# Performance work log

Measured on AMD Instinct MI355X. Metric: run time of the kernel, lower is better.

Reference implementation:

```python
import jax, jax.numpy as jnp
import numpy as np
from jax import lax

BAD = -10000.0
K = 10
W = 512  # window_size


def setup_inputs() -> dict:
    key = jax.random.key(0)
    k1, k2, k3, k4 = jax.random.split(key, 4)
    S, B, P, D, R = 4, 256, 32768, 256, 1000
    return {
        "relation": jax.random.randint(k1, (S, B), 0, R, dtype=jnp.int32),
        "head": jax.random.randint(k2, (S, B), 0, P, dtype=jnp.int32),
        "entity_embedding": jax.random.normal(k3, (S, P, D), dtype=jnp.float32),
        "relation_embedding": jax.random.normal(k4, (R, D), dtype=jnp.float32),
    }


def reference(relation, head, entity_embedding, relation_embedding):
    S, B = relation.shape
    P, D = entity_embedding.shape[1], entity_embedding.shape[2]
    Q = S * B            # total queries after all_gather
    NBEST = K + 1
    n_rep = -(-P // W)   # ceil

    # all_gather of queries across shards (every shard sees all queries)
    rel_all = relation.reshape(-1)                                   # (Q,)
    head_emb_all = entity_embedding[jnp.arange(S)[:, None], head]    # (S,B,D)
    head_emb_all = head_emb_all.reshape(Q, D)
    # DistMult score_tails: <h, r, t> ; fold h*r into one query vector
    qvec = head_emb_all * relation_embedding[rel_all]                # (Q,D)

    init_sc = jnp.full((S, Q, NBEST), BAD, dtype=jnp.float32)
    init_ix = jnp.full((S, Q, NBEST), P, dtype=jnp.int32)

    def step(carry, w):
        sc, ix = carry
        start = w * W
        # local idx of this window, clamped like the torch mask branch
        raw = start + jnp.arange(W, dtype=jnp.int32)                 # (W,)
        valid = raw < P
        slide = jnp.where(valid, raw, P - 1)
        neg = lax.dynamic_slice_in_dim(entity_embedding,
                                       jnp.minimum(start, P - W), W, axis=1)  # (S,W,D)
        scores_w = jnp.einsum('qd,swd->sqw', qvec, neg)              # (S,Q,W)
        scores_w = scores_w + BAD * (~valid).astype(scores_w.dtype)
        all_sc = jnp.concatenate([scores_w, sc], axis=-1)            # (S,Q,W+NBEST)
        all_ix = jnp.concatenate(
            [jnp.broadcast_to(slide, (S, Q, W)), ix], axis=-1)
        top_sc, top_pos = lax.top_k(all_sc, NBEST)
        top_ix = jnp.take_along_axis(all_ix, top_pos, axis=-1)
        return (top_sc, top_ix), None

    (best_sc, best_ix), _ = lax.scan(step, (init_sc, init_ix),
                                     jnp.arange(n_rep, dtype=jnp.int32))

    # all_to_all: (src_shard, dst_shard, bs, nbest) -> (dst, src, bs, nbest)
    best_sc = best_sc.reshape(S, S, B, NBEST).transpose(1, 0, 2, 3)
    best_ix = best_ix.reshape(S, S, B, NBEST).transpose(1, 0, 2, 3)

    # mask out placeholder / padding local indices (shard_counts == P)
    best_sc = best_sc + BAD * (best_ix >= P).astype(best_sc.dtype)

    # shard_and_idx_to_entity: interleaved global ids, padded column for idx==P
    base = jnp.arange(P, dtype=jnp.int32)[None, :] * S \
        + jnp.arange(S, dtype=jnp.int32)[:, None]                    # (S,P)
    table = jnp.concatenate(
        [base, jnp.full((S, 1), -1, dtype=jnp.int32)], axis=1)       # (S,P+1)
    src = jnp.arange(S, dtype=jnp.int32)[None, :, None, None]
    best_gid = table[src, best_ix]                                   # (S,S,B,NBEST)

    # per destination shard: merge the S per-source-shard top-(k+1) lists
    sc_flat = best_sc.transpose(0, 2, 1, 3).reshape(S, B, S * NBEST)
    gid_flat = best_gid.transpose(0, 2, 1, 3).reshape(S, B, S * NBEST)
    topk_sc, topk_pos = lax.top_k(sc_flat, K)                        # (S,B,K)
    topk_gid = jnp.take_along_axis(gid_flat, topk_pos, axis=-1)
    return topk_gid, topk_sc
```

## Files before the change

### kernel.cpp

```cpp
#include <hip/hip_runtime.h>

#define SS 4
#define BB 256
#define PP 32768
#define DD 256
#define QQ 1024
#define NN 131072
#define KTOP 10
#define QTILE 128
#define WQ 32
#define NCHUNK 64
#define CHROWS 2048
#define PANEL 64
#define NPANEL (CHROWS / PANEL)
#define JCH 8
#define MSLOT 20
#define ROWG 33
#define ROWE (ROWG * 8)
#define PANB (PANEL * ROWG * 16)
#define KEYMASK 0xFFFFF800u
#define MWS 132
#define CVB 4096

typedef __attribute__((ext_vector_type(8))) short bf16x8;
typedef __attribute__((ext_vector_type(4))) float f32x4;
typedef __attribute__((ext_vector_type(16))) float f32x16;
typedef __attribute__((ext_vector_type(4))) unsigned int u32x4;

static __device__ __forceinline__ short f2bf(float f) {
    union { float f; unsigned u; } v; v.f = f;
    unsigned r = (v.u + 0x7FFFu + ((v.u >> 16) & 1u)) >> 16;
    return (short)r;
}
static __device__ __forceinline__ bf16x8 cvt8(f32x4 a, f32x4 b) {
    bf16x8 r;
    r[0] = f2bf(a[0]); r[1] = f2bf(a[1]); r[2] = f2bf(a[2]); r[3] = f2bf(a[3]);
    r[4] = f2bf(b[0]); r[5] = f2bf(b[1]); r[6] = f2bf(b[2]); r[7] = f2bf(b[3]);
    return r;
}
static __device__ __forceinline__ unsigned umax(unsigned a, unsigned b) { return a > b ? a : b; }
static __device__ __forceinline__ unsigned umin(unsigned a, unsigned b) { return a < b ? a : b; }

__global__ void prep_kernel(const int* __restrict__ rel, const int* __restrict__ head,
                            const float* __restrict__ E, const float* __restrict__ R,
                            short* __restrict__ Ebf, short* __restrict__ qbf) {
    if (blockIdx.x < CVB) {
        size_t base = ((size_t)blockIdx.x * 256 + threadIdx.x) * 32;
        #pragma unroll
        for (int c = 0; c < 4; c++) {
            f32x4 a = *(const f32x4*)(E + base + c * 8);
            f32x4 b = *(const f32x4*)(E + base + c * 8 + 4);
            *(bf16x8*)(Ebf + base + c * 8) = cvt8(a, b);
        }
    } else {
        int q = blockIdx.x - CVB, d = threadIdx.x;
        int s1 = q >> 8;
        float f = E[((size_t)(s1 * PP + head[q])) * DD + d] * R[(size_t)rel[q] * DD + d];
        qbf[q * DD + d] = f2bf(f);
    }
}

__launch_bounds__(256, 2)
__global__ void score_topk_kernel(const short* __restrict__ Ebf, const short* __restrict__ qbf,
                                  unsigned* __restrict__ parts) {
    __shared__ __align__(16) char smem[2 * PANB];

    const int tid  = threadIdx.x;
    const int wave = tid >> 6;
    const int lane = tid & 63;
    const int lh   = lane >> 5;
    const int ln   = lane & 31;
    const int mtile = blockIdx.x >> 6;
    const int chunk = blockIdx.x & 63;

    short* buf0 = (short*)smem;
    short* buf1 = (short*)(smem + PANB);

    bf16x8 afrag[16];
    {
        const int arow = mtile * QTILE + wave * WQ + ln;
        #pragma unroll
        for (int ks = 0; ks < 16; ks++)
            afrag[ks] = *(const bf16x8*)(qbf + arow * DD + ks * 16 + lh * 8);
    }

    unsigned lst[16][4];
    #pragma unroll
    for (int r = 0; r < 16; r++)
        #pragma unroll
        for (int i = 0; i < 4; i++) lst[r][i] = 0u;

    const int n0c = chunk * CHROWS;

    bf16x8 st[8];
    #pragma unroll
    for (int it = 0; it < 8; it++) {
        int gi = it * 256 + tid, row = gi >> 5, slot = gi & 31;
        st[it] = *(const bf16x8*)(Ebf + (size_t)(n0c + row) * DD + slot * 8);
    }
    #pragma unroll
    for (int it = 0; it < 8; it++) {
        int gi = it * 256 + tid, row = gi >> 5, slot = gi & 31;
        *(bf16x8*)(buf0 + row * ROWE + slot * 8) = st[it];
    }

    for (int p = 0; p < NPANEL; p++) {
        short* bp = (p & 1) ? buf1 : buf0;
        short* bn = (p & 1) ? buf0 : buf1;
        __syncthreads();
        if (p + 1 < NPANEL) {
            const int n1 = n0c + (p + 1) * PANEL;
            #pragma unroll
            for (int it = 0; it < 8; it++) {
                int gi = it * 256 + tid, row = gi >> 5, slot = gi & 31;
                st[it] = *(const bf16x8*)(Ebf + (size_t)(n1 + row) * DD + slot * 8);
            }
        }

        f32x16 acc0, acc1;
        #pragma unroll
        for (int r = 0; r < 16; r++) { acc0[r] = 256.0f; acc1[r] = 256.0f; }
        const short* b0 = bp + ln * ROWE + lh * 8;
        const short* b1 = bp + (32 + ln) * ROWE + lh * 8;
        #pragma unroll
        for (int ks = 0; ks < 16; ks++) {
            bf16x8 x0 = *(const bf16x8*)(b0 + ks * 16);
            bf16x8 x1 = *(const bf16x8*)(b1 + ks * 16);
            acc0 = __builtin_amdgcn_mfma_f32_32x32x16_bf16(afrag[ks], x0, acc0, 0, 0, 0);
            acc1 = __builtin_amdgcn_mfma_f32_32x32x16_bf16(afrag[ks], x1, acc1, 0, 0, 0);
        }

        const unsigned c0 = (unsigned)(p * 64 + ln);
        const unsigned c1 = (unsigned)(p * 64 + 32 + ln);
        #pragma unroll
        for (int r = 0; r < 16; r++) {
            unsigned key = (__float_as_uint(acc0[r]) & KEYMASK) | c0;
            unsigned n0 = umin(umax(key, lst[r][0]), lst[r][1]);
            unsigned n1 = umin(umax(key, lst[r][1]), lst[r][2]);
            unsigned n2 = umin(umax(key, lst[r][2]), lst[r][3]);
            unsigned n3 = umax(key, lst[r][3]);
            lst[r][0] = n0; lst[r][1] = n1; lst[r][2] = n2; lst[r][3] = n3;
        }
        #pragma unroll
        for (int r = 0; r < 16; r++) {
            unsigned key = (__float_as_uint(acc1[r]) & KEYMASK) | c1;
            unsigned n0 = umin(umax(key, lst[r][0]), lst[r][1]);
            unsigned n1 = umin(umax(key, lst[r][1]), lst[r][2]);
            unsigned n2 = umin(umax(key, lst[r][2]), lst[r][3]);
            unsigned n3 = umax(key, lst[r][3]);
            lst[r][0] = n0; lst[r][1] = n1; lst[r][2] = n2; lst[r][3] = n3;
        }

        if (p + 1 < NPANEL) {
            #pragma unroll
            for (int it = 0; it < 8; it++) {
                int gi = it * 256 + tid, row = gi >> 5, slot = gi & 31;
                *(bf16x8*)(bn + row * ROWE + slot * 8) = st[it];
            }
        }
    }

    __syncthreads();
    unsigned* mw = (unsigned*)smem + (size_t)wave * (WQ * MWS);
    #pragma unroll
    for (int r = 0; r < 16; r++) {
        int q = (r & 3) + 8 * (r >> 2) + 4 * lh;
        u32x4 v; v[0] = lst[r][0]; v[1] = lst[r][1]; v[2] = lst[r][2]; v[3] = lst[r][3];
        *(u32x4*)(mw + q * MWS + ln * 4) = v;
    }
    if (lane < 32) {
        unsigned rr[JCH];
        #pragma unroll
        for (int i = 0; i < JCH; i++) rr[i] = 0u;
        #pragma unroll
        for (int j = 0; j < 32; j++) {
            u32x4 v = *(const u32x4*)(mw + lane * MWS + j * 4);
            #pragma unroll
            for (int e = 0; e < 4; e++) {
                unsigned x = v[e];
                unsigned t0 = umin(umax(x, rr[0]), rr[1]);
                unsigned t1 = umin(umax(x, rr[1]), rr[2]);
                unsigned t2 = umin(umax(x, rr[2]), rr[3]);
                unsigned t3 = umin(umax(x, rr[3]), rr[4]);
                unsigned t4 = umin(umax(x, rr[4]), rr[5]);
                unsigned t5 = umin(umax(x, rr[5]), rr[6]);
                unsigned t6 = umin(umax(x, rr[6]), rr[7]);
                unsigned t7 = umax(x, rr[7]);
                rr[0]=t0; rr[1]=t1; rr[2]=t2; rr[3]=t3; rr[4]=t4; rr[5]=t5; rr[6]=t6; rr[7]=t7;
            }
        }
        const int qg = mtile * QTILE + wave * WQ + lane;
        unsigned* dst = parts + ((size_t)qg * NCHUNK + chunk) * JCH;
        #pragma unroll
        for (int i = 0; i < JCH; i++) dst[i] = rr[JCH - 1 - i];
    }
}

__global__ void finalize_kernel(const int* __restrict__ rel, const int* __restrict__ head,
                                const float* __restrict__ E, const float* __restrict__ R,
                                const unsigned* __restrict__ parts, float* __restrict__ out) {
    __shared__ float qv[DD];
    __shared__ int   gl[MSLOT];
    __shared__ float rsc[MSLOT];
    __shared__ int   rgid[MSLOT];

    const int q = blockIdx.x;
    const int tid = threadIdx.x;
    const int wave = tid >> 6, lane = tid & 63;
    const int s1 = q >> 8;

    qv[tid] = E[((size_t)(s1 * PP + head[q])) * DD + tid] * R[(size_t)rel[q] * DD + tid];

    if (wave == 0) {
        unsigned run[JCH];
        const unsigned* src = parts + ((size_t)q * NCHUNK + lane) * JCH;
        #pragma unroll
        for (int j = 0; j < JCH; j++) run[j] = src[j];
        for (int r = 0; r < MSLOT; r++) {
            unsigned best = run[0]; int bl = lane;
            #pragma unroll
            for (int off = 32; off >= 1; off >>= 1) {
                unsigned ob = __shfl_xor(best, off);
                int ol = __shfl_xor(bl, off);
                if (ob > best || (ob == best && ol < bl)) { best = ob; bl = ol; }
            }
            if (lane == bl) {
                int col = (int)(best & 0x7FFu);
                int n = lane * CHROWS + col;
                gl[r] = ((n & (PP - 1)) << 2) | (n >> 15);
                #pragma unroll
                for (int j = 0; j < JCH - 1; j++) run[j] = run[j + 1];
                run[JCH - 1] = 0u;
            }
        }
    }
    __syncthreads();

    f32x4 qq = *(const f32x4*)(qv + lane * 4);
    #pragma unroll
    for (int c = 0; c < MSLOT / 4; c++) {
        int j = wave * (MSLOT / 4) + c;
        int gid = gl[j];
        int n = (gid & 3) * PP + (gid >> 2);
        f32x4 ev = *(const f32x4*)(E + (size_t)n * DD + lane * 4);
        f32x4 p = qq * ev;
        float s = (p[0] + p[1]) + (p[2] + p[3]);
        #pragma unroll
        for (int off = 32; off >= 1; off >>= 1) s += __shfl_xor(s, off);
        if (lane == 0) { rsc[j] = s; rgid[j] = gid; }
    }
    __syncthreads();

    if (tid < 64) {
        float a = (tid < MSLOT) ? rsc[tid] : -1e30f;
        int   g = (tid < MSLOT) ? rgid[tid] : 0;
        for (int r = 0; r < KTOP; r++) {
            float ps = a; int pg = g; int plm = tid;
            #pragma unroll
            for (int off = 32; off >= 1; off >>= 1) {
                float os = __shfl_xor(ps, off);
                int   og = __shfl_xor(pg, off);
                int   ol = __shfl_xor(plm, off);
                if (os > ps || (os == ps && ol < plm)) { ps = os; pg = og; plm = ol; }
            }
            if (tid == 0) {
                out[q * KTOP + r]             = (float)pg;
                out[QQ * KTOP + q * KTOP + r] = ps;
            }
            if (tid == plm) a = -1e30f;
        }
    }
}

extern "C" void kernel_launch(void* const* d_in, const int* in_sizes, int n_in,
                              void* d_out, int out_size, void* d_ws, size_t ws_size,
                              hipStream_t stream) {
    const int*   rel  = (const int*)d_in[0];
    const int*   head = (const int*)d_in[1];
    const float* E    = (const float*)d_in[2];
    const float* R    = (const float*)d_in[3];

    char* ws = (char*)d_ws;
    short* Ebf = (short*)ws;
    short* qbf = (short*)(ws + (size_t)NN * DD * 2);
    unsigned* parts = (unsigned*)(ws + (size_t)NN * DD * 2 + (size_t)QQ * DD * 2);

    prep_kernel<<<dim3(CVB + QQ), dim3(256), 0, stream>>>(rel, head, E, R, Ebf, qbf);
    score_topk_kernel<<<dim3((QQ / QTILE) * NCHUNK), dim3(256), 0, stream>>>(Ebf, qbf, parts);
    finalize_kernel<<<dim3(QQ), dim3(256), 0, stream>>>(rel, head, E, R, parts, (float*)d_out);
}
```

Before: 307.0 us.

## Fuse fp32-to-bf16 entity conversion into the score kernel's panel loads

Drops the separate pass that converted the whole entity table to bf16 in workspace. The score kernel now reads fp32 rows directly and packs them to bf16 by truncation while staging panels into shared memory. This removes a full read plus write of the table and one intermediate buffer. In exchange each of the 8 query-tile blocks per chunk reads twice as many bytes from global memory (fp32 instead of bf16), uses more staging registers, and rounds by truncation instead of round-to-nearest.

```diff
diff --git a/kernel.cpp b/kernel.cpp
--- a/kernel.cpp
+++ b/kernel.cpp
@@ -20,7 +20,6 @@
 #define PANB (PANEL * ROWG * 16)
 #define KEYMASK 0xFFFFF800u
 #define MWS 132
-#define CVB 4096
 
 typedef __attribute__((ext_vector_type(8))) short bf16x8;
 typedef __attribute__((ext_vector_type(4))) float f32x4;
@@ -32,36 +31,29 @@
     unsigned r = (v.u + 0x7FFFu + ((v.u >> 16) & 1u)) >> 16;
     return (short)r;
 }
-static __device__ __forceinline__ bf16x8 cvt8(f32x4 a, f32x4 b) {
-    bf16x8 r;
-    r[0] = f2bf(a[0]); r[1] = f2bf(a[1]); r[2] = f2bf(a[2]); r[3] = f2bf(a[3]);
-    r[4] = f2bf(b[0]); r[5] = f2bf(b[1]); r[6] = f2bf(b[2]); r[7] = f2bf(b[3]);
-    return r;
+static __device__ __forceinline__ unsigned pk2(float lo, float hi) {
+    return (__float_as_uint(hi) & 0xFFFF0000u) | (__float_as_uint(lo) >> 16);
+}
+static __device__ __forceinline__ u32x4 pk8(f32x4 a, f32x4 b) {
+    u32x4 g;
+    g[0] = pk2(a[0], a[1]); g[1] = pk2(a[2], a[3]);
+    g[2] = pk2(b[0], b[1]); g[3] = pk2(b[2], b[3]);
+    return g;
 }
 static __device__ __forceinline__ unsigned umax(unsigned a, unsigned b) { return a > b ? a : b; }
 static __device__ __forceinline__ unsigned umin(unsigned a, unsigned b) { return a < b ? a : b; }
 
-__global__ void prep_kernel(const int* __restrict__ rel, const int* __restrict__ head,
+__global__ void qvec_kernel(const int* __restrict__ rel, const int* __restrict__ head,
                             const float* __restrict__ E, const float* __restrict__ R,
-                            short* __restrict__ Ebf, short* __restrict__ qbf) {
-    if (blockIdx.x < CVB) {
-        size_t base = ((size_t)blockIdx.x * 256 + threadIdx.x) * 32;
-        #pragma unroll
-        for (int c = 0; c < 4; c++) {
-            f32x4 a = *(const f32x4*)(E + base + c * 8);
-            f32x4 b = *(const f32x4*)(E + base + c * 8 + 4);
-            *(bf16x8*)(Ebf + base + c * 8) = cvt8(a, b);
-        }
-    } else {
-        int q = blockIdx.x - CVB, d = threadIdx.x;
-        int s1 = q >> 8;
-        float f = E[((size_t)(s1 * PP + head[q])) * DD + d] * R[(size_t)rel[q] * DD + d];
-        qbf[q * DD + d] = f2bf(f);
-    }
+                            short* __restrict__ qbf) {
+    int q = blockIdx.x, d = threadIdx.x;
+    int s1 = q >> 8;
+    float f = E[((size_t)(s1 * PP + head[q])) * DD + d] * R[(size_t)rel[q] * DD + d];
+    qbf[q * DD + d] = f2bf(f);
 }
 
 __launch_bounds__(256, 2)
-__global__ void score_topk_kernel(const short* __restrict__ Ebf, const short* __restrict__ qbf,
+__global__ void score_topk_kernel(const float* __restrict__ E, const short* __restrict__ qbf,
                                   unsigned* __restrict__ parts) {
     __shared__ __align__(16) char smem[2 * PANB];
 
@@ -92,16 +84,18 @@
 
     const int n0c = chunk * CHROWS;
 
-    bf16x8 st[8];
+    f32x4 sa[8], sb[8];
     #pragma unroll
     for (int it = 0; it < 8; it++) {
         int gi = it * 256 + tid, row = gi >> 5, slot = gi & 31;
-        st[it] = *(const bf16x8*)(Ebf + (size_t)(n0c + row) * DD + slot * 8);
+        const float* src = E + (size_t)(n0c + row) * DD + slot * 8;
+        sa[it] = *(const f32x4*)(src);
+        sb[it] = *(const f32x4*)(src + 4);
     }
     #pragma unroll
     for (int it = 0; it < 8; it++) {
         int gi = it * 256 + tid, row = gi >> 5, slot = gi & 31;
-        *(bf16x8*)(buf0 + row * ROWE + slot * 8) = st[it];
+        *(u32x4*)(buf0 + row * ROWE + slot * 8) = pk8(sa[it], sb[it]);
     }
 
     for (int p = 0; p < NPANEL; p++) {
@@ -113,7 +107,9 @@
             #pragma unroll
             for (int it = 0; it < 8; it++) {
                 int gi = it * 256 + tid, row = gi >> 5, slot = gi & 31;
-                st[it] = *(const bf16x8*)(Ebf + (size_t)(n1 + row) * DD + slot * 8);
+                const float* src = E + (size_t)(n1 + row) * DD + slot * 8;
+                sa[it] = *(const f32x4*)(src);
+                sb[it] = *(const f32x4*)(src + 4);
             }
         }
 
@@ -155,7 +151,7 @@
             #pragma unroll
             for (int it = 0; it < 8; it++) {
                 int gi = it * 256 + tid, row = gi >> 5, slot = gi & 31;
-                *(bf16x8*)(bn + row * ROWE + slot * 8) = st[it];
+                *(u32x4*)(bn + row * ROWE + slot * 8) = pk8(sa[it], sb[it]);
             }
         }
     }
@@ -281,11 +277,10 @@
     const float* R    = (const float*)d_in[3];
 
     char* ws = (char*)d_ws;
-    short* Ebf = (short*)ws;
-    short* qbf = (short*)(ws + (size_t)NN * DD * 2);
-    unsigned* parts = (unsigned*)(ws + (size_t)NN * DD * 2 + (size_t)QQ * DD * 2);
-
-    prep_kernel<<<dim3(CVB + QQ), dim3(256), 0, stream>>>(rel, head, E, R, Ebf, qbf);
-    score_topk_kernel<<<dim3((QQ / QTILE) * NCHUNK), dim3(256), 0, stream>>>(Ebf, qbf, parts);
+    short* qbf = (short*)ws;
+    unsigned* parts = (unsigned*)(ws + (size_t)QQ * DD * 2);
+
+    qvec_kernel<<<dim3(QQ), dim3(DD), 0, stream>>>(rel, head, E, R, qbf);
+    score_topk_kernel<<<dim3((QQ / QTILE) * NCHUNK), dim3(256), 0, stream>>>(E, qbf, parts);
     finalize_kernel<<<dim3(QQ), dim3(256), 0, stream>>>(rel, head, E, R, parts, (float*)d_out);
 }
```

Measured after the change: 349.2 us. +13.7%, slower.
